# Performance work log

Measured on AMD Instinct MI355X. Metric: run time of the kernel, lower is better.

Reference implementation:

```python
import jax, jax.numpy as jnp
from jax import lax
import numpy as np

D_MODEL = 1024
D_INNER = 2048   # expand * d_model
D_STATE = 128
NHEADS = 16
HEADDIM = 128
NGROUPS = 1
D_CONV = 4
CHUNK = 256
CONV_DIM = D_INNER + 2 * NGROUPS * D_STATE  # 2304
DIM_IN_PROJ = 2 * D_INNER + 2 * NGROUPS * D_STATE + NHEADS  # 4368
EPS = 1e-5


def setup_inputs() -> dict:
    key = jax.random.key(0)
    ks = jax.random.split(key, 10)
    u = jax.random.normal(ks[0], (2, 4096, D_MODEL), dtype=jnp.float32)
    W_in = jax.random.normal(ks[1], (DIM_IN_PROJ, D_MODEL), dtype=jnp.float32) * (1.0 / np.sqrt(D_MODEL))
    conv_w = jax.random.normal(ks[2], (CONV_DIM, 1, D_CONV), dtype=jnp.float32) * (1.0 / np.sqrt(D_CONV))
    conv_b = jax.random.normal(ks[3], (CONV_DIM,), dtype=jnp.float32) * 0.02
    # dt init: exp(uniform * (log dt_max - log dt_min) + log dt_min), inverse softplus
    dt = jnp.exp(jax.random.uniform(ks[4], (NHEADS,)) * (np.log(0.02) - np.log(0.001)) + np.log(0.001))
    dt = jnp.clip(dt, 1e-4, None)
    dt_bias = dt + jnp.log(-jnp.expm1(-dt))
    A_log = jnp.log(jax.random.uniform(ks[5], (NHEADS,), minval=1.0, maxval=16.0))
    D = jnp.ones((NHEADS,), dtype=jnp.float32)
    norm_weight = jnp.ones((D_INNER,), dtype=jnp.float32)
    W_out = jax.random.normal(ks[6], (D_MODEL, D_INNER), dtype=jnp.float32) * (1.0 / np.sqrt(D_INNER))
    return {"u": u, "W_in": W_in, "conv_w": conv_w, "conv_b": conv_b,
            "dt_bias": dt_bias, "A_log": A_log, "D": D,
            "norm_weight": norm_weight, "W_out": W_out}


def _segsum(x):
    # x: (..., T) -> (..., T, T); out[i, j] = sum_{k=j+1..i} x_k for j <= i, else -inf
    T = x.shape[-1]
    cs = jnp.cumsum(x, axis=-1)
    seg = cs[..., :, None] - cs[..., None, :]
    mask = jnp.tril(jnp.ones((T, T), dtype=bool))
    return jnp.where(mask, seg, -jnp.inf)


def _mamba2_forward(u, W_in, conv_w, conv_b, dt_bias, A_log, D, norm_weight, W_out):
    b, L, _ = u.shape
    zxbcdt = u @ W_in.T  # (b, L, 4368)
    z = zxbcdt[..., :D_INNER]
    xBC = zxbcdt[..., D_INNER:D_INNER + CONV_DIM]
    dt = zxbcdt[..., D_INNER + CONV_DIM:]  # (b, L, h)

    # causal depthwise conv1d + SiLU
    xBC_t = xBC.transpose(0, 2, 1)  # (b, d, L)
    conv = lax.conv_general_dilated(xBC_t, conv_w, (1,), [(D_CONV - 1, 0)],
                                    feature_group_count=CONV_DIM,
                                    dimension_numbers=("NCW", "OIW", "NCW"))
    xBC = jax.nn.silu((conv + conv_b[None, :, None]).transpose(0, 2, 1))

    x = xBC[..., :D_INNER].reshape(b, L, NHEADS, HEADDIM)
    Bm = xBC[..., D_INNER:D_INNER + D_STATE]          # ngroups = 1
    Cm = xBC[..., D_INNER + D_STATE:]

    dt = jax.nn.softplus(dt + dt_bias)  # (b, L, h)
    A = -jnp.exp(A_log)                 # (h,)

    nc = L // CHUNK
    xc = x.reshape(b, nc, CHUNK, NHEADS, HEADDIM)
    dtc = dt.reshape(b, nc, CHUNK, NHEADS)
    Bc = Bm.reshape(b, nc, CHUNK, D_STATE)
    Cc = Cm.reshape(b, nc, CHUNK, D_STATE)

    dA = (dtc * A).transpose(0, 1, 3, 2)        # (b, c, h, q)
    A_cs = jnp.cumsum(dA, axis=-1)              # (b, c, h, q)
    Lmat = jnp.exp(_segsum(dA))                 # (b, c, h, q, q)
    xdt = xc * dtc[..., None]                   # (b, c, q, h, p)

    # intra-chunk (diagonal block) output
    CB = jnp.einsum("bcqn,bcsn->bcqs", Cc, Bc)
    Y_diag = jnp.einsum("bcqs,bchqs,bcshp->bcqhp", CB, Lmat, xdt)

    # per-chunk final states
    decay_states = jnp.exp(A_cs[..., -1:] - A_cs)  # (b, c, h, q)
    states = jnp.einsum("bcqn,bchq,bcqhp->bchpn", Bc, decay_states, xdt)

    # inter-chunk recurrence over chunk axis (small: nc steps)
    chunk_decay = jnp.exp(A_cs[..., -1])  # (b, c, h)
    def step(carry, inp):
        dec, s = inp
        return carry * dec[..., None, None] + s, carry
    init = jnp.zeros_like(states[:, 0])
    _, prev = lax.scan(step, init,
                       (chunk_decay.transpose(1, 0, 2), states.transpose(1, 0, 2, 3, 4)))
    prev = prev.transpose(1, 0, 2, 3, 4)  # (b, c, h, p, n) state entering each chunk

    Y_off = jnp.einsum("bcqn,bchpn,bchq->bcqhp", Cc, prev, jnp.exp(A_cs))

    y = (Y_diag + Y_off).reshape(b, L, NHEADS, HEADDIM) + D[None, None, :, None] * x
    y = y.reshape(b, L, D_INNER)

    # gated RMSNorm (norm_before_gate=False): norm(y * silu(z)) * weight
    y = y * jax.nn.silu(z)
    y = y * lax.rsqrt(jnp.mean(y * y, axis=-1, keepdims=True) + EPS) * norm_weight

    return y @ W_out.T


def reference(u, W_in, conv_w, conv_b, dt_bias, A_log, D, norm_weight, W_out):
    return _mamba2_forward(u, W_in, conv_w, conv_b, dt_bias, A_log, D, norm_weight, W_out)
```

## Files before the change

kernel.cpp:

```cpp
#include <hip/hip_runtime.h>
#include <hip/hip_bf16.h>
#include <cstddef>
#include <cstdint>

#define D_MODEL     1024
#define D_INNER     2048
#define D_STATE     128
#define NHEADS      16
#define HEADDIM     128
#define D_CONV      4
#define CHUNK       256
#define CONV_DIM    2304
#define DIM_IN_PROJ 4368
#define NPAD_WIN    4608
#define BATCH       2
#define SEQ         4096
#define ROWS        8192
#define NC          16
#define EPS         1e-5f

typedef __hip_bfloat16 bf16;
typedef __attribute__((ext_vector_type(8))) short bf16x8;
typedef __attribute__((ext_vector_type(4))) float f32x4;

__device__ __forceinline__ float sigmoidf_(float x) { return 1.f / (1.f + expf(-x)); }

__device__ __forceinline__ float ldf(const float* p) { return *p; }
__device__ __forceinline__ float ldf(const bf16* p)  { return __bfloat162float(*p); }
__device__ __forceinline__ void  stf(float* p, float v) { *p = v; }
__device__ __forceinline__ void  stf(bf16* p, float v)  { *p = __float2bfloat16(v); }

__device__ __forceinline__ short f2bs(float x) {
    bf16 h = __float2bfloat16(x);
    return __builtin_bit_cast(short, h);
}
__device__ __forceinline__ float bs2f(short s) {
    unsigned int u = ((unsigned int)(unsigned short)s) << 16;
    return __builtin_bit_cast(float, u);
}

#define GLOAD_LDS16(gp, lp) \
    __builtin_amdgcn_global_load_lds((const __attribute__((address_space(1))) unsigned int*)(gp), \
        (__attribute__((address_space(3))) unsigned int*)(lp), 16, 0, 0)

__global__ __launch_bounds__(512, 1) void gemm256_mfma_bt(
    const bf16* __restrict__ A, const bf16* __restrict__ B, bf16* __restrict__ C,
    int M, int N, int K, int lda, int ldb, int ldc, int gx)
{
    __shared__ bf16 As[2][2][256 * 32];
    __shared__ bf16 Bs[2][2][256 * 32];

    const int tid  = threadIdx.x;
    const int lane = tid & 63;
    const int wave = tid >> 6;
    const int wm   = wave >> 2;
    const int wn   = wave & 3;
    const int l15  = lane & 15;
    const int l4   = lane >> 4;

    const int cpx  = (int)gridDim.x >> 3;
    const int wg   = ((int)blockIdx.x & 7) * cpx + ((int)blockIdx.x >> 3);
    const int row0 = (wg / gx) * 256;
    const int col0 = (wg % gx) * 256;

    const int NT = K >> 6;

    f32x4 acc[8][4];
#pragma unroll
    for (int m = 0; m < 8; m++)
#pragma unroll
        for (int n = 0; n < 4; n++) acc[m][n] = (f32x4){0.f, 0.f, 0.f, 0.f};

#define BAR_()  { asm volatile("" ::: "memory"); __builtin_amdgcn_s_barrier(); asm volatile("" ::: "memory"); }
#define VMW0_() asm volatile("s_waitcnt vmcnt(0)" ::: "memory")
#define VMW4_() asm volatile("s_waitcnt vmcnt(4)" ::: "memory")

    auto STAGE_A = [&](int kt, int buf, int kk) {
#pragma unroll
        for (int sw = 0; sw < 2; sw++) {
            int s  = sw * 512 + tid;
            int r  = s >> 2;
            int cg = (s & 3) ^ ((r >> 1) & 3);
            const bf16* src = A + (size_t)(row0 + r) * lda + kt * 64 + kk * 32 + cg * 8;
            GLOAD_LDS16(src, &As[buf][kk][s * 8]);
        }
    };
    auto STAGE_B = [&](int kt, int buf, int kk) {
#pragma unroll
        for (int sw = 0; sw < 2; sw++) {
            int s  = sw * 512 + tid;
            int r  = s >> 2;
            int cg = (s & 3) ^ ((r >> 1) & 3);
            const bf16* src = B + (size_t)(col0 + r) * ldb + kt * 64 + kk * 32 + cg * 8;
            GLOAD_LDS16(src, &Bs[buf][kk][s * 8]);
        }
    };
    auto LOADA = [&](int buf, int mq, int kk, bf16x8* af) {
#pragma unroll
        for (int i = 0; i < 4; i++) {
            int r = wm * 128 + (mq * 4 + i) * 16 + l15;
            af[i] = *reinterpret_cast<const bf16x8*>(
                &As[buf][kk][r * 32 + ((l4 ^ ((r >> 1) & 3)) << 3)]);
        }
    };
    auto LOADB = [&](int buf, int kk, bf16x8* bb) {
#pragma unroll
        for (int n = 0; n < 4; n++) {
            int r = wn * 64 + n * 16 + l15;
            bb[n] = *reinterpret_cast<const bf16x8*>(
                &Bs[buf][kk][r * 32 + ((l4 ^ ((r >> 1) & 3)) << 3)]);
        }
    };
    auto MFMAQ = [&](int mq, bf16x8* af, bf16x8* bb) {
        __builtin_amdgcn_s_setprio(1);
#pragma unroll
        for (int i = 0; i < 4; i++)
#pragma unroll
            for (int n = 0; n < 4; n++)
                acc[mq * 4 + i][n] = __builtin_amdgcn_mfma_f32_16x16x32_bf16(
                    af[i], bb[n], acc[mq * 4 + i][n], 0, 0, 0);
        __builtin_amdgcn_s_setprio(0);
    };

    STAGE_A(0, 0, 0); STAGE_B(0, 0, 0);
    STAGE_A(0, 0, 1); STAGE_B(0, 0, 1);
    VMW0_();
    BAR_();

    bf16x8 af[4], bb[4];
    for (int t = 0; t < NT; t++) {
        const int buf  = t & 1;
        const int nbuf = buf ^ 1;
        const int nk   = (t + 1 < NT) ? t + 1 : 0;
        LOADA(buf, 0, 0, af);
        LOADB(buf, 0, bb);
        STAGE_A(nk, nbuf, 0);
        MFMAQ(0, af, bb);
        LOADA(buf, 1, 0, af);
        STAGE_B(nk, nbuf, 0);
        VMW4_();
        BAR_();
        MFMAQ(1, af, bb);
        LOADA(buf, 0, 1, af);
        LOADB(buf, 1, bb);
        STAGE_A(nk, nbuf, 1);
        MFMAQ(0, af, bb);
        LOADA(buf, 1, 1, af);
        STAGE_B(nk, nbuf, 1);
        VMW4_();
        BAR_();
        MFMAQ(1, af, bb);
    }

#pragma unroll
    for (int m = 0; m < 8; m++) {
        int gr = row0 + wm * 128 + m * 16 + l4 * 4;
#pragma unroll
        for (int n = 0; n < 4; n++) {
            int gc = col0 + wn * 64 + n * 16 + l15;
            if (gc < N) {
#pragma unroll
                for (int j = 0; j < 4; j++)
                    stf(&C[(size_t)(gr + j) * ldc + gc], acc[m][n][j]);
            }
        }
    }
#undef BAR_
#undef VMW0_
#undef VMW4_
}

template<typename TC>
__global__ __launch_bounds__(256) void gemm_mfma_bt(
    const bf16* __restrict__ A, const bf16* __restrict__ B, TC* __restrict__ C,
    int M, int N, int K, int lda, int ldb, int ldc,
    long long sA, long long sB, long long sC)
{
    A += (long long)blockIdx.z * sA;
    B += (long long)blockIdx.z * sB;
    C += (long long)blockIdx.z * sC;

    __shared__ bf16 As[128 * 32];
    __shared__ bf16 Bs[128 * 32];

    const int tid  = threadIdx.x;
    const int lane = tid & 63;
    const int wave = tid >> 6;
    const int wr   = wave >> 1;
    const int wc   = wave & 1;
    const int row0 = blockIdx.y * 128;
    const int col0 = blockIdx.x * 128;
    const int l15  = lane & 15;
    const int l4   = lane >> 4;

    const int srow = tid >> 2;
    const int scol = (tid & 3) * 8;

    f32x4 acc[4][4];
#pragma unroll
    for (int m = 0; m < 4; m++)
#pragma unroll
        for (int n = 0; n < 4; n++) acc[m][n] = (f32x4){0.f, 0.f, 0.f, 0.f};

    for (int k0 = 0; k0 < K; k0 += 32) {
        const bf16* gA0 = A + (size_t)(row0 + srow) * lda + k0 + scol;
        const bf16* gA1 = A + (size_t)(row0 + 64 + srow) * lda + k0 + scol;
        const bf16* gB0 = B + (size_t)(col0 + srow) * ldb + k0 + scol;
        const bf16* gB1 = B + (size_t)(col0 + 64 + srow) * ldb + k0 + scol;
        GLOAD_LDS16(gA0, &As[tid * 8]);
        GLOAD_LDS16(gA1, &As[2048 + tid * 8]);
        GLOAD_LDS16(gB0, &Bs[tid * 8]);
        GLOAD_LDS16(gB1, &Bs[2048 + tid * 8]);
        __syncthreads();

        bf16x8 af[4], bg[4];
#pragma unroll
        for (int m = 0; m < 4; m++) {
            int r = wr * 64 + m * 16 + l15;
            af[m] = *reinterpret_cast<const bf16x8*>(&As[r * 32 + l4 * 8]);
        }
#pragma unroll
        for (int n = 0; n < 4; n++) {
            int r = wc * 64 + n * 16 + l15;
            bg[n] = *reinterpret_cast<const bf16x8*>(&Bs[r * 32 + l4 * 8]);
        }
#pragma unroll
        for (int m = 0; m < 4; m++)
#pragma unroll
            for (int n = 0; n < 4; n++)
                acc[m][n] = __builtin_amdgcn_mfma_f32_16x16x32_bf16(af[m], bg[n], acc[m][n], 0, 0, 0);
        __syncthreads();
    }

#pragma unroll
    for (int m = 0; m < 4; m++) {
        int grb = row0 + wr * 64 + m * 16 + l4 * 4;
#pragma unroll
        for (int n = 0; n < 4; n++) {
            int gc = col0 + wc * 64 + n * 16 + l15;
            if (gc < N) {
#pragma unroll
                for (int j = 0; j < 4; j++) {
                    int gr = grb + j;
                    if (gr < M) stf(&C[(size_t)gr * ldc + gc], acc[m][n][j]);
                }
            }
        }
    }
}

__global__ __launch_bounds__(256) void dt_proj_kernel(
    const float* __restrict__ u, const float* __restrict__ Wdt,
    const float* __restrict__ dt_bias, float* __restrict__ dtsp,
    ushort* __restrict__ ub)
{
    const int wave = threadIdx.x >> 6;
    const int lane = threadIdx.x & 63;
    const int row  = blockIdx.x * 4 + wave;
    const float* urow = u + (size_t)row * D_MODEL;

    float4 uv[4];
#pragma unroll
    for (int w = 0; w < 4; w++)
        uv[w] = *reinterpret_cast<const float4*>(&urow[lane * 4 + w * 256]);

#pragma unroll
    for (int w = 0; w < 4; w++) {
        ushort4 o;
        o.x = (unsigned short)f2bs(uv[w].x);
        o.y = (unsigned short)f2bs(uv[w].y);
        o.z = (unsigned short)f2bs(uv[w].z);
        o.w = (unsigned short)f2bs(uv[w].w);
        *reinterpret_cast<ushort4*>(&ub[(size_t)row * D_MODEL + lane * 4 + w * 256]) = o;
    }

    float acc[NHEADS];
#pragma unroll
    for (int h = 0; h < NHEADS; h++) acc[h] = 0.f;
#pragma unroll
    for (int w = 0; w < 4; w++) {
#pragma unroll
        for (int h = 0; h < NHEADS; h++) {
            float4 wv = *reinterpret_cast<const float4*>(&Wdt[(size_t)h * D_MODEL + lane * 4 + w * 256]);
            acc[h] += uv[w].x * wv.x + uv[w].y * wv.y + uv[w].z * wv.z + uv[w].w * wv.w;
        }
    }
#pragma unroll
    for (int h = 0; h < NHEADS; h++)
#pragma unroll
        for (int off = 32; off > 0; off >>= 1)
            acc[h] += __shfl_xor(acc[h], off, 64);

    float sel = 0.f;
#pragma unroll
    for (int h = 0; h < NHEADS; h++) sel = (lane == h) ? acc[h] : sel;
    if (lane < NHEADS) {
        float x = sel + dt_bias[lane];
        dtsp[(size_t)row * NHEADS + lane] = (x > 20.f) ? x : log1pf(expf(x));
    }
}

__global__ __launch_bounds__(256) void cast_bf16_kernel(
    const float4* __restrict__ src, ushort4* __restrict__ dst, int n4)
{
    int i = blockIdx.x * 256 + threadIdx.x;
    if (i >= n4) return;
    float4 v = src[i];
    ushort4 o;
    o.x = (unsigned short)f2bs(v.x);
    o.y = (unsigned short)f2bs(v.y);
    o.z = (unsigned short)f2bs(v.z);
    o.w = (unsigned short)f2bs(v.w);
    dst[i] = o;
}

__global__ __launch_bounds__(256) void cast_win_kernel(
    const float4* __restrict__ src, ushort4* __restrict__ dst)
{
    int i = blockIdx.x * 256 + threadIdx.x;
    if (i >= NPAD_WIN * D_MODEL / 4) return;
    int row = (i * 4) / D_MODEL;
    ushort4 o = {0, 0, 0, 0};
    if (row < DIM_IN_PROJ) {
        float4 v = src[i];
        o.x = (unsigned short)f2bs(v.x);
        o.y = (unsigned short)f2bs(v.y);
        o.z = (unsigned short)f2bs(v.z);
        o.w = (unsigned short)f2bs(v.w);
    }
    dst[i] = o;
}

__global__ __launch_bounds__(256) void conv_silu_kernel(
    const bf16* __restrict__ zx, const float* __restrict__ cw,
    const float* __restrict__ cb, bf16* __restrict__ xbc)
{
    int idx = blockIdx.x * 256 + threadIdx.x;
    if (idx >= ROWS * (CONV_DIM / 8)) return;
    int c8  = idx % (CONV_DIM / 8);
    int row = idx / (CONV_DIM / 8);
    int c0  = c8 * 8;
    int l   = row & (SEQ - 1);

    float acc[8];
    {
        float4 b0 = *reinterpret_cast<const float4*>(&cb[c0]);
        float4 b1 = *reinterpret_cast<const float4*>(&cb[c0 + 4]);
        acc[0] = b0.x; acc[1] = b0.y; acc[2] = b0.z; acc[3] = b0.w;
        acc[4] = b1.x; acc[5] = b1.y; acc[6] = b1.z; acc[7] = b1.w;
    }
    float4 t[8];
#pragma unroll
    for (int j = 0; j < 8; j++)
        t[j] = *reinterpret_cast<const float4*>(&cw[(size_t)(c0 + j) * D_CONV]);

#pragma unroll
    for (int k = 0; k < D_CONV; k++) {
        int ls = l - (D_CONV - 1) + k;
        if (ls < 0) continue;
        const bf16* zp = zx + (size_t)(row - (D_CONV - 1) + k) * DIM_IN_PROJ + D_INNER + c0;
        bf16x8 v = *reinterpret_cast<const bf16x8*>(zp);
#pragma unroll
        for (int j = 0; j < 8; j++) {
            float tap = (k == 0) ? t[j].x : (k == 1) ? t[j].y : (k == 2) ? t[j].z : t[j].w;
            acc[j] += tap * bs2f(v[j]);
        }
    }
    bf16x8 o;
#pragma unroll
    for (int j = 0; j < 8; j++) {
        float x = acc[j];
        o[j] = f2bs(x * sigmoidf_(x));
    }
    *reinterpret_cast<bf16x8*>(&xbc[(size_t)row * CONV_DIM + c0]) = o;
}

__global__ __launch_bounds__(256) void cumsum_kernel(
    const float* __restrict__ dtsp, const float* __restrict__ A_log,
    float* __restrict__ Acs)
{
    int blk = blockIdx.x;
    int h   = blk % NHEADS;
    int bc  = blk / NHEADS;
    int t   = threadIdx.x;
    int row = bc * CHUNK + t;
    float A = -expf(A_log[h]);
    __shared__ float buf[CHUNK];
    buf[t] = dtsp[(size_t)row * NHEADS + h] * A;
    __syncthreads();
    for (int off = 1; off < CHUNK; off <<= 1) {
        float v = (t >= off) ? buf[t - off] : 0.f;
        __syncthreads();
        buf[t] += v;
        __syncthreads();
    }
    Acs[(size_t)blk * CHUNK + t] = buf[t];
}

__global__ __launch_bounds__(256, 2) void states_mfma_kernel(
    const bf16* __restrict__ xbc, const float* __restrict__ dtsp,
    const float* __restrict__ Acs, float* __restrict__ states)
{
    const int bch  = blockIdx.x;
    const int h    = bch % NHEADS;
    const int bc   = bch / NHEADS;
    const int row0 = bc * CHUNK;
    const int tid  = threadIdx.x;
    const int lane = tid & 63;
    const int wave = tid >> 6;
    const int l15  = lane & 15;
    const int l4   = lane >> 4;

    __shared__ float g[CHUNK];
    __shared__ bf16 xT[128 * 32];
    __shared__ bf16 bT[128 * 32];

    {
        float last = Acs[(size_t)bch * CHUNK + CHUNK - 1];
        float a    = Acs[(size_t)bch * CHUNK + tid];
        g[tid] = dtsp[(size_t)(row0 + tid) * NHEADS + h] * __expf(last - a);
    }

    const int sp0 = (tid & 15) * 8;
    const int ssl = 2 * (tid >> 4);

    f32x4 acc[2][8];
#pragma unroll
    for (int m = 0; m < 2; m++)
#pragma unroll
        for (int n = 0; n < 8; n++) acc[m][n] = (f32x4){0.f, 0.f, 0.f, 0.f};

    for (int q0 = 0; q0 < CHUNK; q0 += 32) {
        __syncthreads();
        {
            const bf16* gx = xbc + (size_t)(row0 + q0 + ssl) * CONV_DIM + h * HEADDIM + sp0;
            bf16x8 v0 = *reinterpret_cast<const bf16x8*>(gx);
            bf16x8 v1 = *reinterpret_cast<const bf16x8*>(gx + CONV_DIM);
            const bf16* gb = xbc + (size_t)(row0 + q0 + ssl) * CONV_DIM + D_INNER + sp0;
            bf16x8 w0 = *reinterpret_cast<const bf16x8*>(gb);
            bf16x8 w1 = *reinterpret_cast<const bf16x8*>(gb + CONV_DIM);
            float g0 = g[q0 + ssl], g1 = g[q0 + ssl + 1];
#pragma unroll
            for (int j = 0; j < 8; j++) {
                unsigned int px = (unsigned short)f2bs(bs2f(v0[j]) * g0) |
                                  ((unsigned int)(unsigned short)f2bs(bs2f(v1[j]) * g1) << 16);
                *reinterpret_cast<unsigned int*>(&xT[(sp0 + j) * 32 + ssl]) = px;
                unsigned int pb = (unsigned short)w0[j] |
                                  ((unsigned int)(unsigned short)w1[j] << 16);
                *reinterpret_cast<unsigned int*>(&bT[(sp0 + j) * 32 + ssl]) = pb;
            }
        }
        __syncthreads();

        bf16x8 af[2], bg[8];
#pragma unroll
        for (int m = 0; m < 2; m++) {
            int p = wave * 32 + m * 16 + l15;
            af[m] = *reinterpret_cast<const bf16x8*>(&xT[p * 32 + l4 * 8]);
        }
#pragma unroll
        for (int n = 0; n < 8; n++) {
            int nn = n * 16 + l15;
            bg[n] = *reinterpret_cast<const bf16x8*>(&bT[nn * 32 + l4 * 8]);
        }
#pragma unroll
        for (int m = 0; m < 2; m++)
#pragma unroll
            for (int n = 0; n < 8; n++)
                acc[m][n] = __builtin_amdgcn_mfma_f32_16x16x32_bf16(af[m], bg[n], acc[m][n], 0, 0, 0);
    }

    float* sp = states + (size_t)bch * HEADDIM * D_STATE;
#pragma unroll
    for (int m = 0; m < 2; m++) {
        int pb = wave * 32 + m * 16 + l4 * 4;
#pragma unroll
        for (int n = 0; n < 8; n++) {
            int nn = n * 16 + l15;
#pragma unroll
            for (int j = 0; j < 4; j++)
                sp[(size_t)(pb + j) * D_STATE + nn] = acc[m][n][j];
        }
    }
}

__global__ __launch_bounds__(256) void chunkscan_kernel(
    float* __restrict__ states, const float* __restrict__ Acs)
{
    int idx = blockIdx.x * 256 + threadIdx.x;
    int pn  = idx % (HEADDIM * D_STATE);
    int bh  = idx / (HEADDIM * D_STATE);
    int h   = bh % NHEADS;
    int b   = bh / NHEADS;
    float carry = 0.f;
    for (int c = 0; c < NC; c++) {
        int bch = (b * NC + c) * NHEADS + h;
        size_t off = (size_t)bch * HEADDIM * D_STATE + pn;
        float s   = states[off];
        states[off] = carry;
        float dec = expf(Acs[(size_t)bch * CHUNK + CHUNK - 1]);
        carry = carry * dec + s;
    }
}

__global__ __launch_bounds__(256, 2) void y_mfma_kernel(
    const bf16* __restrict__ xbc, const float* __restrict__ dtsp,
    const float* __restrict__ Acs, const float* __restrict__ CBm,
    const float* __restrict__ prev, bf16* __restrict__ Y)
{
    const int bch  = blockIdx.x;
    const int h    = bch % NHEADS;
    const int bc   = bch / NHEADS;
    const int row0 = bc * CHUNK;
    const int tid  = threadIdx.x;
    const int lane = tid & 63;
    const int wave = tid >> 6;
    const int l15  = lane & 15;
    const int l4   = lane >> 4;

    __shared__ float sAcs[CHUNK];
    __shared__ float sdt[CHUNK];
    __shared__ bf16 xT[128 * 32];

    sAcs[tid] = Acs[(size_t)bch * CHUNK + tid];
    sdt[tid]  = dtsp[(size_t)(row0 + tid) * NHEADS + h];
    __syncthreads();

    int qb[4]; float aq[4];
#pragma unroll
    for (int m = 0; m < 4; m++) {
        qb[m] = (m * 4 + wave) * 16;
        aq[m] = sAcs[qb[m] + l15];
    }

    f32x4 acc[4][8];
#pragma unroll
    for (int m = 0; m < 4; m++)
#pragma unroll
        for (int n = 0; n < 8; n++) acc[m][n] = (f32x4){0.f, 0.f, 0.f, 0.f};

    const int sp0 = (tid & 15) * 8;
    const int ssl = 2 * (tid >> 4);

    for (int s0 = 0; s0 < CHUNK; s0 += 32) {
        __syncthreads();
        {
            const bf16* gx = xbc + (size_t)(row0 + s0 + ssl) * CONV_DIM + h * HEADDIM + sp0;
            bf16x8 v0 = *reinterpret_cast<const bf16x8*>(gx);
            bf16x8 v1 = *reinterpret_cast<const bf16x8*>(gx + CONV_DIM);
            float d0 = sdt[s0 + ssl], d1 = sdt[s0 + ssl + 1];
#pragma unroll
            for (int j = 0; j < 8; j++) {
                unsigned int px = (unsigned short)f2bs(bs2f(v0[j]) * d0) |
                                  ((unsigned int)(unsigned short)f2bs(bs2f(v1[j]) * d1) << 16);
                *reinterpret_cast<unsigned int*>(&xT[(sp0 + j) * 32 + ssl]) = px;
            }
        }
        __syncthreads();

        bf16x8 bg[8];
#pragma unroll
        for (int n = 0; n < 8; n++)
            bg[n] = *reinterpret_cast<const bf16x8*>(&xT[(n * 16 + l15) * 32 + l4 * 8]);

        f32x4 as0 = *reinterpret_cast<const f32x4*>(&sAcs[s0 + l4 * 8]);
        f32x4 as1 = *reinterpret_cast<const f32x4*>(&sAcs[s0 + l4 * 8 + 4]);

#pragma unroll
        for (int m = 0; m < 4; m++) {
            if (s0 >= qb[m] + 16) continue;
            int q = qb[m] + l15;
            const float* cbp = CBm + ((size_t)bc * CHUNK + q) * CHUNK + s0 + l4 * 8;
            f32x4 c0 = *reinterpret_cast<const f32x4*>(cbp);
            f32x4 c1 = *reinterpret_cast<const f32x4*>(cbp + 4);
            bf16x8 af;
#pragma unroll
            for (int j = 0; j < 8; j++) {
                int s = s0 + l4 * 8 + j;
                float cb = (j < 4) ? c0[j] : c1[j - 4];
                float a  = (j < 4) ? as0[j] : as1[j - 4];
                float w  = (s <= q) ? cb * __expf(aq[m] - a) : 0.f;
                af[j] = f2bs(w);
            }
#pragma unroll
            for (int n = 0; n < 8; n++)
                acc[m][n] = __builtin_amdgcn_mfma_f32_16x16x32_bf16(af, bg[n], acc[m][n], 0, 0, 0);
        }
    }

    float eaq[4];
#pragma unroll
    for (int m = 0; m < 4; m++) eaq[m] = __expf(aq[m]);

    const float* prevh = prev + (size_t)bch * HEADDIM * D_STATE;
    for (int n0 = 0; n0 < D_STATE; n0 += 32) {
        bf16x8 bg[8];
#pragma unroll
        for (int n = 0; n < 8; n++) {
            const float* pr = prevh + (size_t)(n * 16 + l15) * D_STATE + n0 + l4 * 8;
            f32x4 u0 = *reinterpret_cast<const f32x4*>(pr);
            f32x4 u1 = *reinterpret_cast<const f32x4*>(pr + 4);
            bf16x8 b;
#pragma unroll
            for (int j = 0; j < 4; j++) { b[j] = f2bs(u0[j]); b[4 + j] = f2bs(u1[j]); }
            bg[n] = b;
        }
#pragma unroll
        for (int m = 0; m < 4; m++) {
            const bf16* crow = xbc + (size_t)(row0 + qb[m] + l15) * CONV_DIM
                             + D_INNER + D_STATE + n0 + l4 * 8;
            bf16x8 cv = *reinterpret_cast<const bf16x8*>(crow);
            bf16x8 af;
#pragma unroll
            for (int j = 0; j < 8; j++) af[j] = f2bs(bs2f(cv[j]) * eaq[m]);
#pragma unroll
            for (int n = 0; n < 8; n++)
                acc[m][n] = __builtin_amdgcn_mfma_f32_16x16x32_bf16(af, bg[n], acc[m][n], 0, 0, 0);
        }
    }

#pragma unroll
    for (int m = 0; m < 4; m++) {
        int qrb = qb[m] + l4 * 4;
#pragma unroll
        for (int n = 0; n < 8; n++) {
            int p = n * 16 + l15;
#pragma unroll
            for (int j = 0; j < 4; j++)
                stf(&Y[(size_t)(row0 + qrb + j) * D_INNER + h * HEADDIM + p], acc[m][n][j]);
        }
    }
}

__global__ __launch_bounds__(256) void gate_norm_kernel(
    bf16* __restrict__ Yio, const bf16* __restrict__ zx,
    const bf16* __restrict__ xbc, const float* __restrict__ Dv,
    const float* __restrict__ nw)
{
    int row = blockIdx.x;
    int t   = threadIdx.x;
    int d0  = t * 8;

    bf16x8 yv = *reinterpret_cast<const bf16x8*>(&Yio[(size_t)row * D_INNER + d0]);
    bf16x8 xv = *reinterpret_cast<const bf16x8*>(&xbc[(size_t)row * CONV_DIM + d0]);
    bf16x8 zv = *reinterpret_cast<const bf16x8*>(&zx[(size_t)row * DIM_IN_PROJ + d0]);
    float Dh = Dv[d0 >> 7];

    float vals[8];
    float ss = 0.f;
#pragma unroll
    for (int j = 0; j < 8; j++) {
        float y = bs2f(yv[j]) + Dh * bs2f(xv[j]);
        float z = bs2f(zv[j]);
        y *= z * sigmoidf_(z);
        vals[j] = y;
        ss += y * y;
    }
    __shared__ float red[256];
    red[t] = ss;
    __syncthreads();
    for (int o = 128; o > 0; o >>= 1) {
        if (t < o) red[t] += red[t + o];
        __syncthreads();
    }
    float rms = rsqrtf(red[0] / (float)D_INNER + EPS);

    float4 w0 = *reinterpret_cast<const float4*>(&nw[d0]);
    float4 w1 = *reinterpret_cast<const float4*>(&nw[d0 + 4]);
    bf16x8 o;
    o[0] = f2bs(vals[0] * rms * w0.x);
    o[1] = f2bs(vals[1] * rms * w0.y);
    o[2] = f2bs(vals[2] * rms * w0.z);
    o[3] = f2bs(vals[3] * rms * w0.w);
    o[4] = f2bs(vals[4] * rms * w1.x);
    o[5] = f2bs(vals[5] * rms * w1.y);
    o[6] = f2bs(vals[6] * rms * w1.z);
    o[7] = f2bs(vals[7] * rms * w1.w);
    *reinterpret_cast<bf16x8*>(&Yio[(size_t)row * D_INNER + d0]) = o;
}

extern "C" void kernel_launch(void* const* d_in, const int* in_sizes, int n_in,
                              void* d_out, int out_size, void* d_ws, size_t ws_size,
                              hipStream_t stream)
{
    const float* u       = (const float*)d_in[0];
    const float* W_in    = (const float*)d_in[1];
    const float* conv_w  = (const float*)d_in[2];
    const float* conv_b  = (const float*)d_in[3];
    const float* dt_bias = (const float*)d_in[4];
    const float* A_log   = (const float*)d_in[5];
    const float* Dv      = (const float*)d_in[6];
    const float* norm_w  = (const float*)d_in[7];
    const float* W_out   = (const float*)d_in[8];
    float* out = (float*)d_out;

    char* base = (char*)d_ws;
    size_t off = 0;
    auto alloc = [&](size_t bytes) -> char* {
        char* p = base + off;
        off += (bytes + 255) & ~(size_t)255;
        return p;
    };
    bf16*  zxb    = (bf16*) alloc((size_t)ROWS * DIM_IN_PROJ * 2);
    bf16*  xbc    = (bf16*) alloc((size_t)ROWS * CONV_DIM * 2);
    float* dtsp   = (float*)alloc((size_t)ROWS * NHEADS * 4);
    float* Acs    = (float*)alloc((size_t)BATCH * NC * NHEADS * CHUNK * 4);
    float* states = (float*)alloc((size_t)BATCH * NC * NHEADS * HEADDIM * D_STATE * 4);
    float* CBm    = (float*)alloc((size_t)BATCH * NC * CHUNK * CHUNK * 4);
    bf16*  Y      = (bf16*) alloc((size_t)ROWS * D_INNER * 2);
    bf16*  woutb  = (bf16*) alloc((size_t)D_MODEL * D_INNER * 2);
    bf16*  ub     = Y;
    bf16*  winb   = Y + (size_t)ROWS * D_MODEL;
    if (off > ws_size) return;

    dt_proj_kernel<<<ROWS / 4, 256, 0, stream>>>(
        u, W_in + (size_t)(D_INNER + CONV_DIM) * D_MODEL, dt_bias, dtsp, (ushort*)ub);

    cast_win_kernel<<<(NPAD_WIN * D_MODEL / 4 + 255) / 256, 256, 0, stream>>>(
        (const float4*)W_in, (ushort4*)winb);
    cast_bf16_kernel<<<(D_MODEL * D_INNER / 4 + 255) / 256, 256, 0, stream>>>(
        (const float4*)W_out, (ushort4*)woutb, D_MODEL * D_INNER / 4);

    gemm256_mfma_bt<<<(ROWS / 256) * (NPAD_WIN / 256), 512, 0, stream>>>(
        ub, winb, zxb, ROWS, DIM_IN_PROJ, D_MODEL,
        D_MODEL, D_MODEL, DIM_IN_PROJ, NPAD_WIN / 256);

    conv_silu_kernel<<<(ROWS * (CONV_DIM / 8)) / 256, 256, 0, stream>>>(
        zxb, conv_w, conv_b, xbc);

    cumsum_kernel<<<BATCH * NC * NHEADS, 256, 0, stream>>>(dtsp, A_log, Acs);

    states_mfma_kernel<<<BATCH * NC * NHEADS, 256, 0, stream>>>(xbc, dtsp, Acs, states);

    chunkscan_kernel<<<(BATCH * NHEADS * HEADDIM * D_STATE) / 256, 256, 0, stream>>>(
        states, Acs);

    gemm_mfma_bt<float><<<dim3(2, 2, BATCH * NC), 256, 0, stream>>>(
        xbc + D_INNER + D_STATE, xbc + D_INNER, CBm,
        CHUNK, CHUNK, D_STATE, CONV_DIM, CONV_DIM, CHUNK,
        (long long)CHUNK * CONV_DIM, (long long)CHUNK * CONV_DIM, (long long)CHUNK * CHUNK);

    y_mfma_kernel<<<BATCH * NC * NHEADS, 256, 0, stream>>>(xbc, dtsp, Acs, CBm, states, Y);

    gate_norm_kernel<<<ROWS, 256, 0, stream>>>(Y, zxb, xbc, Dv, norm_w);

    gemm_mfma_bt<float><<<dim3(D_MODEL / 128, ROWS / 128, 1), 256, 0, stream>>>(
        Y, woutb, out, ROWS, D_MODEL, D_INNER, D_INNER, D_INNER, D_MODEL, 0, 0, 0);
}
```

Before: 411.7 us.

## Shrink in-proj GEMM to 128x128 tiles and reuse it for out-proj

The 256x256, 512-thread in-projection GEMM becomes a templated 128x128, 256-thread kernel with two blocks per CU. The same kernel, with XCD-aware block swizzling and direct-to-LDS staging, now also runs the output projection in place of the generic gemm_mfma_bt. The aim is more blocks for better CU occupancy and load balance on the in-projection, and a faster pipelined kernel for the out-projection. Smaller tiles give less data reuse per block, so operand traffic rises.

```diff
diff --git a/kernel.cpp b/kernel.cpp
--- a/kernel.cpp
+++ b/kernel.cpp
@@ -43,31 +43,32 @@
     __builtin_amdgcn_global_load_lds((const __attribute__((address_space(1))) unsigned int*)(gp), \
         (__attribute__((address_space(3))) unsigned int*)(lp), 16, 0, 0)
 
-__global__ __launch_bounds__(512, 1) void gemm256_mfma_bt(
-    const bf16* __restrict__ A, const bf16* __restrict__ B, bf16* __restrict__ C,
+template<typename TC>
+__global__ __launch_bounds__(256, 2) void gemm128c_mfma_bt(
+    const bf16* __restrict__ A, const bf16* __restrict__ B, TC* __restrict__ C,
     int M, int N, int K, int lda, int ldb, int ldc, int gx)
 {
-    __shared__ bf16 As[2][2][256 * 32];
-    __shared__ bf16 Bs[2][2][256 * 32];
+    __shared__ bf16 As[2][2][128 * 32];
+    __shared__ bf16 Bs[2][2][128 * 32];
 
     const int tid  = threadIdx.x;
     const int lane = tid & 63;
     const int wave = tid >> 6;
-    const int wm   = wave >> 2;
-    const int wn   = wave & 3;
+    const int wm   = wave >> 1;
+    const int wn   = wave & 1;
     const int l15  = lane & 15;
     const int l4   = lane >> 4;
 
     const int cpx  = (int)gridDim.x >> 3;
     const int wg   = ((int)blockIdx.x & 7) * cpx + ((int)blockIdx.x >> 3);
-    const int row0 = (wg / gx) * 256;
-    const int col0 = (wg % gx) * 256;
+    const int row0 = (wg / gx) * 128;
+    const int col0 = (wg % gx) * 128;
 
     const int NT = K >> 6;
 
-    f32x4 acc[8][4];
-#pragma unroll
-    for (int m = 0; m < 8; m++)
+    f32x4 acc[4][4];
+#pragma unroll
+    for (int m = 0; m < 4; m++)
 #pragma unroll
         for (int n = 0; n < 4; n++) acc[m][n] = (f32x4){0.f, 0.f, 0.f, 0.f};
 
@@ -78,7 +79,7 @@
     auto STAGE_A = [&](int kt, int buf, int kk) {
 #pragma unroll
         for (int sw = 0; sw < 2; sw++) {
-            int s  = sw * 512 + tid;
+            int s  = sw * 256 + tid;
             int r  = s >> 2;
             int cg = (s & 3) ^ ((r >> 1) & 3);
             const bf16* src = A + (size_t)(row0 + r) * lda + kt * 64 + kk * 32 + cg * 8;
@@ -88,17 +89,17 @@
     auto STAGE_B = [&](int kt, int buf, int kk) {
 #pragma unroll
         for (int sw = 0; sw < 2; sw++) {
-            int s  = sw * 512 + tid;
+            int s  = sw * 256 + tid;
             int r  = s >> 2;
             int cg = (s & 3) ^ ((r >> 1) & 3);
             const bf16* src = B + (size_t)(col0 + r) * ldb + kt * 64 + kk * 32 + cg * 8;
             GLOAD_LDS16(src, &Bs[buf][kk][s * 8]);
         }
     };
-    auto LOADA = [&](int buf, int mq, int kk, bf16x8* af) {
+    auto LOADA = [&](int buf, int kk, bf16x8* af) {
 #pragma unroll
         for (int i = 0; i < 4; i++) {
-            int r = wm * 128 + (mq * 4 + i) * 16 + l15;
+            int r = wm * 64 + i * 16 + l15;
             af[i] = *reinterpret_cast<const bf16x8*>(
                 &As[buf][kk][r * 32 + ((l4 ^ ((r >> 1) & 3)) << 3)]);
         }
@@ -111,14 +112,14 @@
                 &Bs[buf][kk][r * 32 + ((l4 ^ ((r >> 1) & 3)) << 3)]);
         }
     };
-    auto MFMAQ = [&](int mq, bf16x8* af, bf16x8* bb) {
+    auto MFMAQ = [&](bf16x8* af, bf16x8* bb) {
         __builtin_amdgcn_s_setprio(1);
 #pragma unroll
         for (int i = 0; i < 4; i++)
 #pragma unroll
             for (int n = 0; n < 4; n++)
-                acc[mq * 4 + i][n] = __builtin_amdgcn_mfma_f32_16x16x32_bf16(
-                    af[i], bb[n], acc[mq * 4 + i][n], 0, 0, 0);
+                acc[i][n] = __builtin_amdgcn_mfma_f32_16x16x32_bf16(
+                    af[i], bb[n], acc[i][n], 0, 0, 0);
         __builtin_amdgcn_s_setprio(0);
     };
 
@@ -132,29 +133,25 @@
         const int buf  = t & 1;
         const int nbuf = buf ^ 1;
         const int nk   = (t + 1 < NT) ? t + 1 : 0;
-        LOADA(buf, 0, 0, af);
+        LOADA(buf, 0, af);
         LOADB(buf, 0, bb);
         STAGE_A(nk, nbuf, 0);
-        MFMAQ(0, af, bb);
-        LOADA(buf, 1, 0, af);
         STAGE_B(nk, nbuf, 0);
         VMW4_();
         BAR_();
-        MFMAQ(1, af, bb);
-        LOADA(buf, 0, 1, af);
+        MFMAQ(af, bb);
+        LOADA(buf, 1, af);
         LOADB(buf, 1, bb);
         STAGE_A(nk, nbuf, 1);
-        MFMAQ(0, af, bb);
-        LOADA(buf, 1, 1, af);
         STAGE_B(nk, nbuf, 1);
         VMW4_();
         BAR_();
-        MFMAQ(1, af, bb);
-    }
-
-#pragma unroll
-    for (int m = 0; m < 8; m++) {
-        int gr = row0 + wm * 128 + m * 16 + l4 * 4;
+        MFMAQ(af, bb);
+    }
+
+#pragma unroll
+    for (int m = 0; m < 4; m++) {
+        int gr = row0 + wm * 64 + m * 16 + l4 * 4;
 #pragma unroll
         for (int n = 0; n < 4; n++) {
             int gc = col0 + wn * 64 + n * 16 + l15;
@@ -721,9 +718,9 @@
     cast_bf16_kernel<<<(D_MODEL * D_INNER / 4 + 255) / 256, 256, 0, stream>>>(
         (const float4*)W_out, (ushort4*)woutb, D_MODEL * D_INNER / 4);
 
-    gemm256_mfma_bt<<<(ROWS / 256) * (NPAD_WIN / 256), 512, 0, stream>>>(
+    gemm128c_mfma_bt<bf16><<<(ROWS / 128) * (NPAD_WIN / 128), 256, 0, stream>>>(
         ub, winb, zxb, ROWS, DIM_IN_PROJ, D_MODEL,
-        D_MODEL, D_MODEL, DIM_IN_PROJ, NPAD_WIN / 256);
+        D_MODEL, D_MODEL, DIM_IN_PROJ, NPAD_WIN / 128);
 
     conv_silu_kernel<<<(ROWS * (CONV_DIM / 8)) / 256, 256, 0, stream>>>(
         zxb, conv_w, conv_b, xbc);
@@ -744,6 +741,6 @@
 
     gate_norm_kernel<<<ROWS, 256, 0, stream>>>(Y, zxb, xbc, Dv, norm_w);
 
-    gemm_mfma_bt<float><<<dim3(D_MODEL / 128, ROWS / 128, 1), 256, 0, stream>>>(
-        Y, woutb, out, ROWS, D_MODEL, D_INNER, D_INNER, D_INNER, D_MODEL, 0, 0, 0);
-}
+    gemm128c_mfma_bt<float><<<(ROWS / 128) * (D_MODEL / 128), 256, 0, stream>>>(
+        Y, woutb, out, ROWS, D_MODEL, D_INNER, D_INNER, D_INNER, D_MODEL, D_MODEL / 128);
+}
```

Measured after the change: 397.7 us. 1.04x faster.

## Add pipelined direct-to-LDS out-projection GEMM and row-blocked conv1d

Applied to the files above, without the earlier changes.

Adds a new 128x128 GEMM kernel for the output projection. It double-buffers LDS with direct global-to-LDS loads, XOR-swizzles LDS to avoid bank conflicts, raises MFMA priority, uses a K step of 64, and remaps blocks across XCDs. It replaces the older gemm_mfma_bt call for the W_out projection. Separately, the conv+SiLU kernel now computes 4 consecutive rows per thread and reuses 7 loaded input rows instead of loading 4 taps per row. The costs are higher register use and a quarter as many conv threads.

```diff
diff --git a/kernel.cpp b/kernel.cpp
--- a/kernel.cpp
+++ b/kernel.cpp
@@ -171,6 +171,130 @@
 }
 
 template<typename TC>
+__global__ __launch_bounds__(256, 2) void gemm128c_mfma_bt(
+    const bf16* __restrict__ A, const bf16* __restrict__ B, TC* __restrict__ C,
+    int M, int N, int K, int lda, int ldb, int ldc, int gx)
+{
+    __shared__ bf16 As[2][2][128 * 32];
+    __shared__ bf16 Bs[2][2][128 * 32];
+
+    const int tid  = threadIdx.x;
+    const int lane = tid & 63;
+    const int wave = tid >> 6;
+    const int wm   = wave >> 1;
+    const int wn   = wave & 1;
+    const int l15  = lane & 15;
+    const int l4   = lane >> 4;
+
+    const int cpx  = (int)gridDim.x >> 3;
+    const int wg   = ((int)blockIdx.x & 7) * cpx + ((int)blockIdx.x >> 3);
+    const int row0 = (wg / gx) * 128;
+    const int col0 = (wg % gx) * 128;
+
+    const int NT = K >> 6;
+
+    f32x4 acc[4][4];
+#pragma unroll
+    for (int m = 0; m < 4; m++)
+#pragma unroll
+        for (int n = 0; n < 4; n++) acc[m][n] = (f32x4){0.f, 0.f, 0.f, 0.f};
+
+#define BAR_()  { asm volatile("" ::: "memory"); __builtin_amdgcn_s_barrier(); asm volatile("" ::: "memory"); }
+#define VMW0_() asm volatile("s_waitcnt vmcnt(0)" ::: "memory")
+#define VMW4_() asm volatile("s_waitcnt vmcnt(4)" ::: "memory")
+
+    auto STAGE_A = [&](int kt, int buf, int kk) {
+#pragma unroll
+        for (int sw = 0; sw < 2; sw++) {
+            int s  = sw * 256 + tid;
+            int r  = s >> 2;
+            int cg = (s & 3) ^ ((r >> 1) & 3);
+            const bf16* src = A + (size_t)(row0 + r) * lda + kt * 64 + kk * 32 + cg * 8;
+            GLOAD_LDS16(src, &As[buf][kk][s * 8]);
+        }
+    };
+    auto STAGE_B = [&](int kt, int buf, int kk) {
+#pragma unroll
+        for (int sw = 0; sw < 2; sw++) {
+            int s  = sw * 256 + tid;
+            int r  = s >> 2;
+            int cg = (s & 3) ^ ((r >> 1) & 3);
+            const bf16* src = B + (size_t)(col0 + r) * ldb + kt * 64 + kk * 32 + cg * 8;
+            GLOAD_LDS16(src, &Bs[buf][kk][s * 8]);
+        }
+    };
+    auto LOADA = [&](int buf, int kk, bf16x8* af) {
+#pragma unroll
+        for (int i = 0; i < 4; i++) {
+            int r = wm * 64 + i * 16 + l15;
+            af[i] = *reinterpret_cast<const bf16x8*>(
+                &As[buf][kk][r * 32 + ((l4 ^ ((r >> 1) & 3)) << 3)]);
+        }
+    };
+    auto LOADB = [&](int buf, int kk, bf16x8* bb) {
+#pragma unroll
+        for (int n = 0; n < 4; n++) {
+            int r = wn * 64 + n * 16 + l15;
+            bb[n] = *reinterpret_cast<const bf16x8*>(
+                &Bs[buf][kk][r * 32 + ((l4 ^ ((r >> 1) & 3)) << 3)]);
+        }
+    };
+    auto MFMAQ = [&](bf16x8* af, bf16x8* bb) {
+        __builtin_amdgcn_s_setprio(1);
+#pragma unroll
+        for (int i = 0; i < 4; i++)
+#pragma unroll
+            for (int n = 0; n < 4; n++)
+                acc[i][n] = __builtin_amdgcn_mfma_f32_16x16x32_bf16(
+                    af[i], bb[n], acc[i][n], 0, 0, 0);
+        __builtin_amdgcn_s_setprio(0);
+    };
+
+    STAGE_A(0, 0, 0); STAGE_B(0, 0, 0);
+    STAGE_A(0, 0, 1); STAGE_B(0, 0, 1);
+    VMW0_();
+    BAR_();
+
+    bf16x8 af[4], bb[4];
+    for (int t = 0; t < NT; t++) {
+        const int buf  = t & 1;
+        const int nbuf = buf ^ 1;
+        const int nk   = (t + 1 < NT) ? t + 1 : 0;
+        LOADA(buf, 0, af);
+        LOADB(buf, 0, bb);
+        STAGE_A(nk, nbuf, 0);
+        STAGE_B(nk, nbuf, 0);
+        VMW4_();
+        BAR_();
+        MFMAQ(af, bb);
+        LOADA(buf, 1, af);
+        LOADB(buf, 1, bb);
+        STAGE_A(nk, nbuf, 1);
+        STAGE_B(nk, nbuf, 1);
+        VMW4_();
+        BAR_();
+        MFMAQ(af, bb);
+    }
+
+#pragma unroll
+    for (int m = 0; m < 4; m++) {
+        int gr = row0 + wm * 64 + m * 16 + l4 * 4;
+#pragma unroll
+        for (int n = 0; n < 4; n++) {
+            int gc = col0 + wn * 64 + n * 16 + l15;
+            if (gc < N) {
+#pragma unroll
+                for (int j = 0; j < 4; j++)
+                    stf(&C[(size_t)(gr + j) * ldc + gc], acc[m][n][j]);
+            }
+        }
+    }
+#undef BAR_
+#undef VMW0_
+#undef VMW4_
+}
+
+template<typename TC>
 __global__ __launch_bounds__(256) void gemm_mfma_bt(
     const bf16* __restrict__ A, const bf16* __restrict__ B, TC* __restrict__ C,
     int M, int N, int K, int lda, int ldb, int ldc,
@@ -335,44 +459,63 @@
     const bf16* __restrict__ zx, const float* __restrict__ cw,
     const float* __restrict__ cb, bf16* __restrict__ xbc)
 {
+    const int CW = CONV_DIM / 8;
     int idx = blockIdx.x * 256 + threadIdx.x;
-    if (idx >= ROWS * (CONV_DIM / 8)) return;
-    int c8  = idx % (CONV_DIM / 8);
-    int row = idx / (CONV_DIM / 8);
-    int c0  = c8 * 8;
-    int l   = row & (SEQ - 1);
-
-    float acc[8];
+    if (idx >= (ROWS / 4) * CW) return;
+    int c8   = idx % CW;
+    int r4   = idx / CW;
+    int c0   = c8 * 8;
+    int row0 = r4 * 4;
+    int l0   = row0 & (SEQ - 1);
+
+    float vr[7][8];
+#pragma unroll
+    for (int k = 0; k < 7; k++) {
+        int ls = l0 - 3 + k;
+        if (ls < 0) {
+#pragma unroll
+            for (int j = 0; j < 8; j++) vr[k][j] = 0.f;
+        } else {
+            bf16x8 v = *reinterpret_cast<const bf16x8*>(
+                zx + (size_t)(row0 - 3 + k) * DIM_IN_PROJ + D_INNER + c0);
+#pragma unroll
+            for (int j = 0; j < 8; j++) vr[k][j] = bs2f(v[j]);
+        }
+    }
+
+    float4 t[8];
+#pragma unroll
+    for (int j = 0; j < 8; j++)
+        t[j] = *reinterpret_cast<const float4*>(&cw[(size_t)(c0 + j) * D_CONV]);
+    float bias[8];
     {
         float4 b0 = *reinterpret_cast<const float4*>(&cb[c0]);
         float4 b1 = *reinterpret_cast<const float4*>(&cb[c0 + 4]);
-        acc[0] = b0.x; acc[1] = b0.y; acc[2] = b0.z; acc[3] = b0.w;
-        acc[4] = b1.x; acc[5] = b1.y; acc[6] = b1.z; acc[7] = b1.w;
-    }
-    float4 t[8];
-#pragma unroll
-    for (int j = 0; j < 8; j++)
-        t[j] = *reinterpret_cast<const float4*>(&cw[(size_t)(c0 + j) * D_CONV]);
-
-#pragma unroll
-    for (int k = 0; k < D_CONV; k++) {
-        int ls = l - (D_CONV - 1) + k;
-        if (ls < 0) continue;
-        const bf16* zp = zx + (size_t)(row - (D_CONV - 1) + k) * DIM_IN_PROJ + D_INNER + c0;
-        bf16x8 v = *reinterpret_cast<const bf16x8*>(zp);
+        bias[0] = b0.x; bias[1] = b0.y; bias[2] = b0.z; bias[3] = b0.w;
+        bias[4] = b1.x; bias[5] = b1.y; bias[6] = b1.z; bias[7] = b1.w;
+    }
+
+#pragma unroll
+    for (int r = 0; r < 4; r++) {
+        float acc[8];
+#pragma unroll
+        for (int j = 0; j < 8; j++) acc[j] = bias[j];
+#pragma unroll
+        for (int k = 0; k < D_CONV; k++) {
+#pragma unroll
+            for (int j = 0; j < 8; j++) {
+                float tap = (k == 0) ? t[j].x : (k == 1) ? t[j].y : (k == 2) ? t[j].z : t[j].w;
+                acc[j] += tap * vr[r + k][j];
+            }
+        }
+        bf16x8 o;
 #pragma unroll
         for (int j = 0; j < 8; j++) {
-            float tap = (k == 0) ? t[j].x : (k == 1) ? t[j].y : (k == 2) ? t[j].z : t[j].w;
-            acc[j] += tap * bs2f(v[j]);
-        }
-    }
-    bf16x8 o;
-#pragma unroll
-    for (int j = 0; j < 8; j++) {
-        float x = acc[j];
-        o[j] = f2bs(x * sigmoidf_(x));
-    }
-    *reinterpret_cast<bf16x8*>(&xbc[(size_t)row * CONV_DIM + c0]) = o;
+            float x = acc[j];
+            o[j] = f2bs(x * sigmoidf_(x));
+        }
+        *reinterpret_cast<bf16x8*>(&xbc[(size_t)(row0 + r) * CONV_DIM + c0]) = o;
+    }
 }
 
 __global__ __launch_bounds__(256) void cumsum_kernel(
@@ -725,7 +868,7 @@
         ub, winb, zxb, ROWS, DIM_IN_PROJ, D_MODEL,
         D_MODEL, D_MODEL, DIM_IN_PROJ, NPAD_WIN / 256);
 
-    conv_silu_kernel<<<(ROWS * (CONV_DIM / 8)) / 256, 256, 0, stream>>>(
+    conv_silu_kernel<<<((ROWS / 4) * (CONV_DIM / 8)) / 256, 256, 0, stream>>>(
         zxb, conv_w, conv_b, xbc);
 
     cumsum_kernel<<<BATCH * NC * NHEADS, 256, 0, stream>>>(dtsp, A_log, Acs);
@@ -744,6 +887,6 @@
 
     gate_norm_kernel<<<ROWS, 256, 0, stream>>>(Y, zxb, xbc, Dv, norm_w);
 
-    gemm_mfma_bt<float><<<dim3(D_MODEL / 128, ROWS / 128, 1), 256, 0, stream>>>(
-        Y, woutb, out, ROWS, D_MODEL, D_INNER, D_INNER, D_INNER, D_MODEL, 0, 0, 0);
-}
+    gemm128c_mfma_bt<float><<<(ROWS / 128) * (D_MODEL / 128), 256, 0, stream>>>(
+        Y, woutb, out, ROWS, D_MODEL, D_INNER, D_INNER, D_INNER, D_MODEL, D_MODEL / 128);
+}
```

Measured after the change: 336.5 us. 18.3% less time.
